# Optimization experiments

Hardware: AMD Instinct MI355X
Metric: run time of the kernel (lower is better)

Reference implementation:

```python
import jax, jax.numpy as jnp
import numpy as np

N = 50000
E = 600000
IN1, IN2, HID, OUT = 256, 128, 128, 64


def gcn_conv(x, W, b, src, dst, n):
    """PyG GCNConv: D^{-1/2}(A+I)D^{-1/2} X W + b with self-loops."""
    h = x @ W  # [N, F_out]
    # degree including self-loop (edge weight 1)
    deg = jax.ops.segment_sum(jnp.ones_like(dst, dtype=h.dtype), dst, num_segments=n) + 1.0
    dinv = deg ** -0.5
    coef = dinv[src] * dinv[dst]  # [E]
    agg = jax.ops.segment_sum(h[src] * coef[:, None], dst, num_segments=n)
    agg = agg + h * (dinv * dinv)[:, None]  # self-loop contribution
    return agg + b


def gcn_stack(x, edge_index, Ws, bs, n):
    src, dst = edge_index[0], edge_index[1]
    x = jax.nn.relu(gcn_conv(x, Ws[0], bs[0], src, dst, n))
    return gcn_conv(x, Ws[1], bs[1], src, dst, n)


def setup_inputs() -> dict:
    key = jax.random.key(0)
    ks = jax.random.split(key, 12)
    glorot = lambda k, fi, fo: jax.random.normal(k, (fi, fo), jnp.float32) * np.sqrt(2.0 / (fi + fo))
    return {
        "x1": jax.random.normal(ks[0], (N, IN1), jnp.float32),
        "edge_index1": jax.random.randint(ks[1], (2, E), 0, N, jnp.int32),
        "x2": jax.random.normal(ks[2], (N, IN2), jnp.float32),
        "edge_index2": jax.random.randint(ks[3], (2, E), 0, N, jnp.int32),
        "W1_0": glorot(ks[4], IN1, HID), "b1_0": jnp.zeros((HID,), jnp.float32),
        "W1_1": glorot(ks[5], HID, OUT), "b1_1": jnp.zeros((OUT,), jnp.float32),
        "W2_0": glorot(ks[6], IN2, HID), "b2_0": jnp.zeros((HID,), jnp.float32),
        "W2_1": glorot(ks[7], HID, OUT), "b2_1": jnp.zeros((OUT,), jnp.float32),
    }


def reference(x1, edge_index1, x2, edge_index2,
              W1_0, b1_0, W1_1, b1_1, W2_0, b2_0, W2_1, b2_1):
    out1 = gcn_stack(x1, edge_index1, (W1_0, W1_1), (b1_0, b1_1), N)
    out2 = gcn_stack(x2, edge_index2, (W2_0, W2_1), (b2_0, b2_1), N)
    return out1, out2
```

## Files before the change

### kernel.cpp

```cpp
#include <hip/hip_runtime.h>
#include <hip/hip_bf16.h>
#include <cstdint>
#include <type_traits>

static constexpr int NN = 50000;
static constexpr int NE = 600000;
static constexpr int NB = (NN + 255) / 256;
static constexpr int CHUNK = 1024;
static constexpr int NCH = (NE + CHUNK - 1) / CHUNK;
static constexpr int CAP = 4096;

typedef __bf16 bf16;
typedef __attribute__((ext_vector_type(2))) __bf16 bf16x2;
typedef __attribute__((ext_vector_type(8))) __bf16 bf16x8;
typedef __attribute__((ext_vector_type(4))) float f32x4;

__global__ __launch_bounds__(256) void k_wprep4(const float* __restrict__ WA,
                                                const float* __restrict__ WB,
                                                const float* __restrict__ WC,
                                                const float* __restrict__ WD,
                                                bf16* __restrict__ wf0,
                                                bf16* __restrict__ wf1,
                                                int* __restrict__ bucketcur,
                                                int* __restrict__ row_off) {
    int y = blockIdx.y;
    int i = blockIdx.x * 256 + threadIdx.x;
    if (y == 4) {
        if (i < 2 * NB) bucketcur[i] = i * CAP;
        if (i < 2) row_off[i * (NN + 1) + NN] = NE;
        return;
    }
    const float* W = (y == 0) ? WA : (y == 1) ? WB : (y == 2) ? WC : WD;
    bf16* wf = (y == 0) ? wf0 : (y == 1) ? wf0 + 256 * 128 : (y == 2) ? wf1 : wf1 + 128 * 64;
    int K = (y == 0) ? 256 : 128;
    int F = (y <= 1) ? 128 : 64;
    if (i < K * F) {
        int k = i / F, n = i % F;
        wf[((size_t)(k >> 3) * F + n) * 8 + (k & 7)] = (bf16)W[i];
    }
}

template <int K, int F, typename AT>
__device__ __forceinline__ void gemm_body(const AT* __restrict__ X,
                                          const bf16* __restrict__ wf,
                                          bf16* __restrict__ H, int n, int bx) {
    constexpr int NT = F / 16;
    int wave = threadIdx.x >> 6;
    int lane = threadIdx.x & 63;
    int lm = lane & 15;
    int lk = lane >> 4;
    int r0 = bx * 64 + wave * 16;

    int arow = r0 + lm;
    if (arow >= n) arow = n - 1;
    const AT* xrow = X + (size_t)arow * K;

    f32x4 acc[NT] = {};

    for (int k0 = 0; k0 < K; k0 += 32) {
        bf16x8 af;
        if constexpr (std::is_same_v<AT, float>) {
            f32x4 a0 = *reinterpret_cast<const f32x4*>(xrow + k0 + lk * 8);
            f32x4 a1 = *reinterpret_cast<const f32x4*>(xrow + k0 + lk * 8 + 4);
            af[0] = (bf16)a0.x; af[1] = (bf16)a0.y; af[2] = (bf16)a0.z; af[3] = (bf16)a0.w;
            af[4] = (bf16)a1.x; af[5] = (bf16)a1.y; af[6] = (bf16)a1.z; af[7] = (bf16)a1.w;
        } else {
            af = *reinterpret_cast<const bf16x8*>(xrow + k0 + lk * 8);
        }
        const bf16* wbase = wf + ((size_t)(k0 / 8 + lk) * F) * 8;
        #pragma unroll
        for (int t = 0; t < NT; ++t) {
            bf16x8 bfg = *reinterpret_cast<const bf16x8*>(wbase + (t * 16 + lm) * 8);
            acc[t] = __builtin_amdgcn_mfma_f32_16x16x32_bf16(af, bfg, acc[t], 0, 0, 0);
        }
    }

    #pragma unroll
    for (int t = 0; t < NT; ++t) {
        #pragma unroll
        for (int i = 0; i < 4; ++i) {
            int gr = r0 + lk * 4 + i;
            if (gr < n) H[(size_t)gr * F + t * 16 + lm] = (bf16)acc[t][i];
        }
    }
}

static constexpr int GB = (NN + 63) / 64;

__global__ __launch_bounds__(256) void k_mega(const float* __restrict__ x1,
                                              const float* __restrict__ x2,
                                              const bf16* __restrict__ wf0,
                                              bf16* __restrict__ h,
                                              const int* __restrict__ srcA,
                                              const int* __restrict__ dstA,
                                              const int* __restrict__ srcB,
                                              const int* __restrict__ dstB,
                                              int* __restrict__ bucketcur,
                                              int2* __restrict__ stg) {
    __shared__ int2 sorted[CHUNK];
    __shared__ int cnt[NB];
    __shared__ int lbase[NB];
    __shared__ int ibase[NB];
    int bx = blockIdx.x;
    if (bx >= 2 * NCH) {
        int gx = bx - 2 * NCH;
        if (gx < GB)
            gemm_body<256, 128, float>(x1, wf0, h, NN, gx);
        else
            gemm_body<128, 128, float>(x2, wf0 + 256 * 128, h + (size_t)NN * 128, NN, gx - GB);
        return;
    }
    int g = (bx >= NCH);
    int chunk = bx - g * NCH;
    const int* src = g ? srcB : srcA;
    const int* dst = g ? dstB : dstA;
    int tid = threadIdx.x;
    int c0 = chunk * CHUNK;
    int total = min(CHUNK, NE - c0);

    if (tid < NB) cnt[tid] = 0;
    __syncthreads();
    #pragma unroll
    for (int it = 0; it < CHUNK / 256; ++it) {
        int e = c0 + it * 256 + tid;
        if (e < NE) atomicAdd(&cnt[dst[e] >> 8], 1);
    }
    __syncthreads();
    int* s = reinterpret_cast<int*>(sorted);
    int v = (tid < NB) ? cnt[tid] : 0;
    s[tid] = v;
    __syncthreads();
    for (int off = 1; off < 256; off <<= 1) {
        int t = (tid >= off) ? s[tid - off] : 0;
        __syncthreads();
        s[tid] += t;
        __syncthreads();
    }
    int incl = s[tid];
    __syncthreads();
    if (tid < NB) {
        lbase[tid] = incl - v;
        ibase[tid] = v ? atomicAdd(&bucketcur[g * NB + tid], v) : 0;
        cnt[tid] = 0;
    }
    __syncthreads();
    #pragma unroll
    for (int it = 0; it < CHUNK / 256; ++it) {
        int e = c0 + it * 256 + tid;
        if (e < NE) {
            int sv = src[e], d = dst[e];
            int b = d >> 8;
            int p = atomicAdd(&cnt[b], 1);
            sorted[lbase[b] + p] = make_int2(sv, d);
        }
    }
    __syncthreads();
    for (int p = tid; p < total; p += 256) {
        int2 sd = sorted[p];
        int b = sd.y >> 8;
        stg[(size_t)ibase[b] + (p - lbase[b])] = sd;
    }
}

__global__ __launch_bounds__(256) void k_binB1(const int2* __restrict__ stg,
                                               const int* __restrict__ bucketcur,
                                               int* __restrict__ row_off,
                                               float* __restrict__ dinv) {
    __shared__ int cnt[256];
    __shared__ int s[256];
    __shared__ int bb[256];
    int g = blockIdx.y;
    int b = blockIdx.x;
    int B = g * NB + b;
    int tid = threadIdx.x;

    int cv = (tid < NB) ? bucketcur[g * NB + tid] - (g * NB + tid) * CAP : 0;
    s[tid] = cv;
    __syncthreads();
    for (int off = 1; off < 256; off <<= 1) {
        int t = (tid >= off) ? s[tid - off] : 0;
        __syncthreads();
        s[tid] += t;
        __syncthreads();
    }
    if (tid < NB) bb[tid] = s[tid] - cv;
    cnt[tid] = 0;
    __syncthreads();
    int base = bb[b];

    int node0 = b << 8;
    int nnod = min(256, NN - node0);
    int count = bucketcur[B] - B * CAP;
    const int2* s0 = stg + (size_t)B * CAP;
    for (int j = tid; j < count; j += 256)
        atomicAdd(&cnt[s0[j].y - node0], 1);
    __syncthreads();
    int v = cnt[tid];
    s[tid] = v;
    __syncthreads();
    for (int off = 1; off < 256; off <<= 1) {
        int t = (tid >= off) ? s[tid - off] : 0;
        __syncthreads();
        s[tid] += t;
        __syncthreads();
    }
    if (tid < nnod) {
        row_off[g * (NN + 1) + node0 + tid] = base + s[tid] - v;
        dinv[(size_t)g * NN + node0 + tid] = rsqrtf((float)v + 1.0f);
    }
}

__global__ __launch_bounds__(256) void k_binB2(const int2* __restrict__ stg,
                                               const int* __restrict__ bucketcur,
                                               const int* __restrict__ row_off,
                                               const float* __restrict__ dinv,
                                               int2* __restrict__ pair) {
    __shared__ int lcur[256];
    __shared__ float ldv[256];
    int g = blockIdx.y;
    int b = blockIdx.x;
    int B = g * NB + b;
    int tid = threadIdx.x;
    int node0 = b << 8;
    int nnod = min(256, NN - node0);
    const int* ro = row_off + g * (NN + 1);
    if (tid < nnod) {
        lcur[tid] = ro[node0 + tid];
        ldv[tid] = dinv[(size_t)g * NN + node0 + tid];
    }
    __syncthreads();
    int count = bucketcur[B] - B * CAP;
    const int2* s0 = stg + (size_t)B * CAP;
    for (int j = tid; j < count; j += 256) {
        int2 sd = s0[j];
        int rel = sd.y - node0;
        int pos = atomicAdd(&lcur[rel], 1);
        float cf = dinv[(size_t)g * NN + sd.x] * ldv[rel];
        pair[(size_t)g * NE + pos] = make_int2(sd.x << 8, __float_as_int(cf));
    }
}

__global__ __launch_bounds__(256) void gemm_l2(const bf16* __restrict__ a,
                                               const bf16* __restrict__ wf1,
                                               bf16* __restrict__ h2) {
    int bx = blockIdx.x;
    int g = (bx >= GB);
    gemm_body<128, 64, bf16>(a + (size_t)g * NN * 128, wf1 + g * 128 * 64,
                             h2 + (size_t)g * NN * 64, NN, bx - g * GB);
}

__global__ __launch_bounds__(256) void agg128_2(const bf16* __restrict__ hb,
                                                const int* __restrict__ row_off,
                                                const int2* __restrict__ pairb,
                                                const float* __restrict__ dinv,
                                                const float* __restrict__ biasA,
                                                const float* __restrict__ biasB,
                                                bf16* __restrict__ ab) {
    int wid = blockIdx.x * 4 + (threadIdx.x >> 6);
    if (wid >= 2 * NN) return;
    int g = (wid >= NN);
    int node = wid - g * NN;
    int lane = threadIdx.x & 63;

    const bf16* h = hb + (size_t)g * NN * 128;
    const char* hB = reinterpret_cast<const char*>(h);
    const int2* pair = pairb + (size_t)g * NE;
    const int* ro = row_off + g * (NN + 1);
    const float* bias = g ? biasB : biasA;

    int f = lane * 2;
    int fb = lane * 4;
    float di = dinv[g * NN + node];
    int beg = ro[node];
    int end = ro[node + 1];

    float a0 = 0.f, a1 = 0.f;

    auto edge1 = [&](int2 p) {
        float c = __int_as_float(p.y);
        bf16x2 v = *reinterpret_cast<const bf16x2*>(hB + (unsigned)p.x + fb);
        a0 = fmaf((float)v[0], c, a0); a1 = fmaf((float)v[1], c, a1);
    };
    auto edge2 = [&](int4 q) {
        float cA = __int_as_float(q.y), cB = __int_as_float(q.w);
        bf16x2 vA = *reinterpret_cast<const bf16x2*>(hB + (unsigned)q.x + fb);
        bf16x2 vB = *reinterpret_cast<const bf16x2*>(hB + (unsigned)q.z + fb);
        a0 = fmaf((float)vA[0], cA, a0); a1 = fmaf((float)vA[1], cA, a1);
        a0 = fmaf((float)vB[0], cB, a0); a1 = fmaf((float)vB[1], cB, a1);
    };

    int j = beg;
    if ((j & 1) && j < end) { edge1(pair[j]); ++j; }
    for (; j + 7 < end; j += 8) {
        int4 q0 = *reinterpret_cast<const int4*>(&pair[j]);
        int4 q1 = *reinterpret_cast<const int4*>(&pair[j + 2]);
        int4 q2 = *reinterpret_cast<const int4*>(&pair[j + 4]);
        int4 q3 = *reinterpret_cast<const int4*>(&pair[j + 6]);
        edge2(q0); edge2(q1); edge2(q2); edge2(q3);
    }
    for (; j + 1 < end; j += 2) {
        int4 q = *reinterpret_cast<const int4*>(&pair[j]);
        edge2(q);
    }
    if (j < end) edge1(pair[j]);

    bf16x2 hv = *reinterpret_cast<const bf16x2*>(&h[(size_t)node * 128 + f]);
    float sc = di * di;
    a0 = fmaf((float)hv[0], sc, a0) + bias[f];
    a1 = fmaf((float)hv[1], sc, a1) + bias[f + 1];
    a0 = fmaxf(a0, 0.f);
    a1 = fmaxf(a1, 0.f);

    bf16x2 r;
    r[0] = (bf16)a0; r[1] = (bf16)a1;
    *reinterpret_cast<bf16x2*>(&ab[((size_t)g * NN + node) * 128 + f]) = r;
}

__global__ __launch_bounds__(256) void agg64_2(const bf16* __restrict__ h2b,
                                               const int* __restrict__ row_off,
                                               const int2* __restrict__ pairb,
                                               const float* __restrict__ dinv,
                                               const float* __restrict__ biasA,
                                               const float* __restrict__ biasB,
                                               float* __restrict__ outb) {
    int wid = blockIdx.x * 4 + (threadIdx.x >> 6);
    if (wid >= 2 * NN) return;
    int g = (wid >= NN);
    int node = wid - g * NN;
    int lane = threadIdx.x & 63;

    const bf16* h = h2b + (size_t)g * NN * 64;
    const char* hB = reinterpret_cast<const char*>(h);
    const int2* pair = pairb + (size_t)g * NE;
    const int* ro = row_off + g * (NN + 1);
    const float* bias = g ? biasB : biasA;
    float* out = outb + (size_t)g * NN * 64;

    int half = lane >> 5;
    int f = (lane & 31) * 2;
    int fb = (lane & 31) * 4;
    float di = dinv[(size_t)g * NN + node];
    int beg = ro[node];
    int end = ro[node + 1];

    float a0 = 0.f, a1 = 0.f;

    auto edge = [&](int2 p) {
        float c = __int_as_float(p.y);
        bf16x2 v = *reinterpret_cast<const bf16x2*>(hB + (((unsigned)p.x) >> 1) + fb);
        a0 = fmaf((float)v[0], c, a0); a1 = fmaf((float)v[1], c, a1);
    };

    int j = beg;
    for (; j + 7 < end; j += 8) {
        int2 p0 = pair[j + half], p1 = pair[j + 2 + half];
        int2 p2 = pair[j + 4 + half], p3 = pair[j + 6 + half];
        edge(p0); edge(p1); edge(p2); edge(p3);
    }
    for (; j + 1 < end; j += 2) edge(pair[j + half]);
    if (j < end && half == 0) edge(pair[j]);

    a0 += __shfl_xor(a0, 32);
    a1 += __shfl_xor(a1, 32);

    bf16x2 hv = *reinterpret_cast<const bf16x2*>(&h[(size_t)node * 64 + f]);
    float sc = di * di;
    a0 = fmaf((float)hv[0], sc, a0) + bias[f];
    a1 = fmaf((float)hv[1], sc, a1) + bias[f + 1];

    if (half == 0) {
        out[(size_t)node * 64 + f] = a0;
        out[(size_t)node * 64 + f + 1] = a1;
    }
}

extern "C" void kernel_launch(void* const* d_in, const int* in_sizes, int n_in,
                              void* d_out, int out_size, void* d_ws, size_t ws_size,
                              hipStream_t stream) {
    const float* x1 = (const float*)d_in[0];
    const int* ei1 = (const int*)d_in[1];
    const float* x2 = (const float*)d_in[2];
    const int* ei2 = (const int*)d_in[3];
    const float* W1_0 = (const float*)d_in[4];
    const float* b1_0 = (const float*)d_in[5];
    const float* W1_1 = (const float*)d_in[6];
    const float* b1_1 = (const float*)d_in[7];
    const float* W2_0 = (const float*)d_in[8];
    const float* b2_0 = (const float*)d_in[9];
    const float* W2_1 = (const float*)d_in[10];
    const float* b2_1 = (const float*)d_in[11];

    float* out = (float*)d_out;

    char* ws = (char*)d_ws;
    size_t off = 0;
    auto alloc = [&](size_t bytes) {
        size_t o = off;
        off = (off + bytes + 255) & ~(size_t)255;
        return o;
    };
    bf16* h = (bf16*)(ws + alloc((size_t)2 * NN * 128 * 2));
    size_t r2 = (size_t)2 * NB * CAP * 8;
    char* region2 = ws + alloc(r2);
    int2* stg = (int2*)region2;
    bf16* h2 = (bf16*)region2;
    bf16* a = (bf16*)(ws + alloc((size_t)2 * NN * 128 * 2));
    int2* pair = (int2*)(ws + alloc((size_t)2 * NE * 8));
    int* row_off = (int*)(ws + alloc((size_t)2 * (NN + 1) * 4));
    float* dinv = (float*)(ws + alloc((size_t)2 * NN * 4));
    int* bucketcur = (int*)(ws + alloc((size_t)2 * NB * 4));
    bf16* wf0 = (bf16*)(ws + alloc((size_t)2 * 256 * 128 * 2));
    bf16* wf1 = (bf16*)(ws + alloc((size_t)2 * 128 * 64 * 2));

    const int* srcA = ei1, *dstA = ei1 + NE;
    const int* srcB = ei2, *dstB = ei2 + NE;

    k_wprep4<<<dim3(128, 5), 256, 0, stream>>>(W1_0, W2_0, W1_1, W2_1, wf0, wf1,
                                               bucketcur, row_off);
    k_mega<<<2 * NCH + 2 * GB, 256, 0, stream>>>(x1, x2, wf0, h,
                                                 srcA, dstA, srcB, dstB, bucketcur, stg);
    k_binB1<<<dim3(NB, 2), 256, 0, stream>>>(stg, bucketcur, row_off, dinv);
    k_binB2<<<dim3(NB, 2), 256, 0, stream>>>(stg, bucketcur, row_off, dinv, pair);

    agg128_2<<<(2 * NN + 3) / 4, 256, 0, stream>>>(h, row_off, pair, dinv, b1_0, b2_0, a);
    gemm_l2<<<2 * GB, 256, 0, stream>>>(a, wf1, h2);
    agg64_2<<<(2 * NN + 3) / 4, 256, 0, stream>>>(h2, row_off, pair, dinv, b1_1, b2_1, out);
}
```

Baseline: 188.4 us.

## Replace atomic bucket cursors with fixed-capacity per-chunk cells and a scan

Result: slower. 209.3 us (+11.1%).

```diff
diff --git a/kernel.cpp b/kernel.cpp
--- a/kernel.cpp
+++ b/kernel.cpp
@@ -6,9 +6,9 @@
 static constexpr int NN = 50000;
 static constexpr int NE = 600000;
 static constexpr int NB = (NN + 255) / 256;
-static constexpr int CHUNK = 1024;
+static constexpr int CHUNK = 2048;
 static constexpr int NCH = (NE + CHUNK - 1) / CHUNK;
-static constexpr int CAP = 4096;
+static constexpr int CCAP = 40;
 
 typedef __bf16 bf16;
 typedef __attribute__((ext_vector_type(2))) __bf16 bf16x2;
@@ -21,12 +21,10 @@
                                                 const float* __restrict__ WD,
                                                 bf16* __restrict__ wf0,
                                                 bf16* __restrict__ wf1,
-                                                int* __restrict__ bucketcur,
                                                 int* __restrict__ row_off) {
     int y = blockIdx.y;
     int i = blockIdx.x * 256 + threadIdx.x;
     if (y == 4) {
-        if (i < 2 * NB) bucketcur[i] = i * CAP;
         if (i < 2) row_off[i * (NN + 1) + NN] = NE;
         return;
     }
@@ -95,12 +93,11 @@
                                               const int* __restrict__ dstA,
                                               const int* __restrict__ srcB,
                                               const int* __restrict__ dstB,
-                                              int* __restrict__ bucketcur,
+                                              int* __restrict__ cellcnt,
                                               int2* __restrict__ stg) {
     __shared__ int2 sorted[CHUNK];
     __shared__ int cnt[NB];
     __shared__ int lbase[NB];
-    __shared__ int ibase[NB];
     int bx = blockIdx.x;
     if (bx >= 2 * NCH) {
         int gx = bx - 2 * NCH;
@@ -140,7 +137,7 @@
     __syncthreads();
     if (tid < NB) {
         lbase[tid] = incl - v;
-        ibase[tid] = v ? atomicAdd(&bucketcur[g * NB + tid], v) : 0;
+        cellcnt[(size_t)(g * NB + tid) * NCH + chunk] = v;
         cnt[tid] = 0;
     }
     __syncthreads();
@@ -158,24 +155,54 @@
     for (int p = tid; p < total; p += 256) {
         int2 sd = sorted[p];
         int b = sd.y >> 8;
-        stg[(size_t)ibase[b] + (p - lbase[b])] = sd;
-    }
+        stg[((size_t)(g * NB + b) * NCH + chunk) * CCAP + (p - lbase[b])] = sd;
+    }
+}
+
+__global__ __launch_bounds__(256) void k_cellscan(const int* __restrict__ cellcnt,
+                                                  int* __restrict__ bucket_base) {
+    __shared__ int s[256];
+    int g = blockIdx.x;
+    int tid = threadIdx.x;
+    int tot = 0;
+    if (tid < NB) {
+        const int* row = cellcnt + (size_t)(g * NB + tid) * NCH;
+        for (int c = 0; c < NCH; ++c) tot += row[c];
+    }
+    s[tid] = tot;
+    __syncthreads();
+    for (int off = 1; off < 256; off <<= 1) {
+        int t = (tid >= off) ? s[tid - off] : 0;
+        __syncthreads();
+        s[tid] += t;
+        __syncthreads();
+    }
+    if (tid < NB) bucket_base[g * NB + tid] = s[tid] - tot;
 }
 
 __global__ __launch_bounds__(256) void k_binB1(const int2* __restrict__ stg,
-                                               const int* __restrict__ bucketcur,
+                                               const int* __restrict__ cellcnt,
+                                               const int* __restrict__ bucket_base,
                                                int* __restrict__ row_off,
                                                float* __restrict__ dinv) {
-    __shared__ int cnt[256];
+    __shared__ int deg[256];
     __shared__ int s[256];
-    __shared__ int bb[256];
     int g = blockIdx.y;
     int b = blockIdx.x;
     int B = g * NB + b;
     int tid = threadIdx.x;
-
-    int cv = (tid < NB) ? bucketcur[g * NB + tid] - (g * NB + tid) * CAP : 0;
-    s[tid] = cv;
+    int node0 = b << 8;
+    int nnod = min(256, NN - node0);
+    deg[tid] = 0;
+    __syncthreads();
+    for (int c = tid; c < NCH; c += 256) {
+        int n = cellcnt[(size_t)B * NCH + c];
+        const int2* cs = stg + ((size_t)B * NCH + c) * CCAP;
+        for (int i = 0; i < n; ++i) atomicAdd(&deg[cs[i].y - node0], 1);
+    }
+    __syncthreads();
+    int v = deg[tid];
+    s[tid] = v;
     __syncthreads();
     for (int off = 1; off < 256; off <<= 1) {
         int t = (tid >= off) ? s[tid - off] : 0;
@@ -183,35 +210,14 @@
         s[tid] += t;
         __syncthreads();
     }
-    if (tid < NB) bb[tid] = s[tid] - cv;
-    cnt[tid] = 0;
-    __syncthreads();
-    int base = bb[b];
-
-    int node0 = b << 8;
-    int nnod = min(256, NN - node0);
-    int count = bucketcur[B] - B * CAP;
-    const int2* s0 = stg + (size_t)B * CAP;
-    for (int j = tid; j < count; j += 256)
-        atomicAdd(&cnt[s0[j].y - node0], 1);
-    __syncthreads();
-    int v = cnt[tid];
-    s[tid] = v;
-    __syncthreads();
-    for (int off = 1; off < 256; off <<= 1) {
-        int t = (tid >= off) ? s[tid - off] : 0;
-        __syncthreads();
-        s[tid] += t;
-        __syncthreads();
-    }
     if (tid < nnod) {
-        row_off[g * (NN + 1) + node0 + tid] = base + s[tid] - v;
+        row_off[g * (NN + 1) + node0 + tid] = bucket_base[B] + s[tid] - v;
         dinv[(size_t)g * NN + node0 + tid] = rsqrtf((float)v + 1.0f);
     }
 }
 
 __global__ __launch_bounds__(256) void k_binB2(const int2* __restrict__ stg,
-                                               const int* __restrict__ bucketcur,
+                                               const int* __restrict__ cellcnt,
                                                const int* __restrict__ row_off,
                                                const float* __restrict__ dinv,
                                                int2* __restrict__ pair) {
@@ -229,14 +235,16 @@
         ldv[tid] = dinv[(size_t)g * NN + node0 + tid];
     }
     __syncthreads();
-    int count = bucketcur[B] - B * CAP;
-    const int2* s0 = stg + (size_t)B * CAP;
-    for (int j = tid; j < count; j += 256) {
-        int2 sd = s0[j];
-        int rel = sd.y - node0;
-        int pos = atomicAdd(&lcur[rel], 1);
-        float cf = dinv[(size_t)g * NN + sd.x] * ldv[rel];
-        pair[(size_t)g * NE + pos] = make_int2(sd.x << 8, __float_as_int(cf));
+    for (int c = tid; c < NCH; c += 256) {
+        int n = cellcnt[(size_t)B * NCH + c];
+        const int2* cs = stg + ((size_t)B * NCH + c) * CCAP;
+        for (int i = 0; i < n; ++i) {
+            int2 sd = cs[i];
+            int rel = sd.y - node0;
+            int pos = atomicAdd(&lcur[rel], 1);
+            float cf = dinv[(size_t)g * NN + sd.x] * ldv[rel];
+            pair[(size_t)g * NE + pos] = make_int2(sd.x << 8, __float_as_int(cf));
+        }
     }
 }
 
@@ -399,28 +407,31 @@
         off = (off + bytes + 255) & ~(size_t)255;
         return o;
     };
-    bf16* h = (bf16*)(ws + alloc((size_t)2 * NN * 128 * 2));
-    size_t r2 = (size_t)2 * NB * CAP * 8;
-    char* region2 = ws + alloc(r2);
-    int2* stg = (int2*)region2;
-    bf16* h2 = (bf16*)region2;
-    bf16* a = (bf16*)(ws + alloc((size_t)2 * NN * 128 * 2));
+    size_t hsz = (size_t)2 * NN * 128 * 2;
+    size_t stg_sz = (size_t)2 * NB * NCH * CCAP * 8;
+    char* R1 = ws + alloc(hsz);
+    bf16* h = (bf16*)R1;
+    bf16* h2 = (bf16*)R1;
+    char* R2 = ws + alloc(stg_sz > hsz ? stg_sz : hsz);
+    int2* stg = (int2*)R2;
+    bf16* a = (bf16*)R2;
     int2* pair = (int2*)(ws + alloc((size_t)2 * NE * 8));
     int* row_off = (int*)(ws + alloc((size_t)2 * (NN + 1) * 4));
     float* dinv = (float*)(ws + alloc((size_t)2 * NN * 4));
-    int* bucketcur = (int*)(ws + alloc((size_t)2 * NB * 4));
+    int* cellcnt = (int*)(ws + alloc((size_t)2 * NB * NCH * 4));
+    int* bucket_base = (int*)(ws + alloc((size_t)2 * NB * 4));
     bf16* wf0 = (bf16*)(ws + alloc((size_t)2 * 256 * 128 * 2));
     bf16* wf1 = (bf16*)(ws + alloc((size_t)2 * 128 * 64 * 2));
 
     const int* srcA = ei1, *dstA = ei1 + NE;
     const int* srcB = ei2, *dstB = ei2 + NE;
 
-    k_wprep4<<<dim3(128, 5), 256, 0, stream>>>(W1_0, W2_0, W1_1, W2_1, wf0, wf1,
-                                               bucketcur, row_off);
+    k_wprep4<<<dim3(128, 5), 256, 0, stream>>>(W1_0, W2_0, W1_1, W2_1, wf0, wf1, row_off);
     k_mega<<<2 * NCH + 2 * GB, 256, 0, stream>>>(x1, x2, wf0, h,
-                                                 srcA, dstA, srcB, dstB, bucketcur, stg);
-    k_binB1<<<dim3(NB, 2), 256, 0, stream>>>(stg, bucketcur, row_off, dinv);
-    k_binB2<<<dim3(NB, 2), 256, 0, stream>>>(stg, bucketcur, row_off, dinv, pair);
+                                                 srcA, dstA, srcB, dstB, cellcnt, stg);
+    k_cellscan<<<2, 256, 0, stream>>>(cellcnt, bucket_base);
+    k_binB1<<<dim3(NB, 2), 256, 0, stream>>>(stg, cellcnt, bucket_base, row_off, dinv);
+    k_binB2<<<dim3(NB, 2), 256, 0, stream>>>(stg, cellcnt, row_off, dinv, pair);
 
     agg128_2<<<(2 * NN + 3) / 4, 256, 0, stream>>>(h, row_off, pair, dinv, b1_0, b2_0, a);
     gemm_l2<<<2 * GB, 256, 0, stream>>>(a, wf1, h2);
```
